# Kernel optimization log

Hardware: AMD Instinct MI355X
Metric: run time of the kernel (lower is better)

The kernel has to match this reference:

```python
import jax, jax.numpy as jnp
import numpy as np

RES = 128
NUM_SAMPLES = 64
EPS = 1e-8


def _trilinear_sample(vol, pts_norm):
    """Trilinear sample of vol [D,H,W] (D=H=W=RES) at pts_norm [N,3] in [-1,1],
    matching F.grid_sample(mode='bilinear', padding_mode='zeros', align_corners=True).
    pts_norm[...,0]=x indexes W, [...,1]=y indexes H, [...,2]=z indexes D."""
    R = vol.shape[0]
    flat = vol.reshape(-1)
    coords = (pts_norm + 1.0) * 0.5 * (R - 1)  # align_corners=True mapping
    x, y, z = coords[:, 0], coords[:, 1], coords[:, 2]
    x0 = jnp.floor(x); y0 = jnp.floor(y); z0 = jnp.floor(z)
    fx = x - x0; fy = y - y0; fz = z - z0

    def corner(xi, yi, zi, w):
        valid = (xi >= 0) & (xi < R) & (yi >= 0) & (yi < R) & (zi >= 0) & (zi < R)
        xc = jnp.clip(xi, 0, R - 1).astype(jnp.int32)
        yc = jnp.clip(yi, 0, R - 1).astype(jnp.int32)
        zc = jnp.clip(zi, 0, R - 1).astype(jnp.int32)
        vals = jnp.take(flat, zc * (R * R) + yc * R + xc)
        return jnp.where(valid, vals * w, 0.0)

    out = corner(x0, y0, z0, (1 - fx) * (1 - fy) * (1 - fz))
    out += corner(x0 + 1, y0, z0, fx * (1 - fy) * (1 - fz))
    out += corner(x0, y0 + 1, z0, (1 - fx) * fy * (1 - fz))
    out += corner(x0 + 1, y0 + 1, z0, fx * fy * (1 - fz))
    out += corner(x0, y0, z0 + 1, (1 - fx) * (1 - fy) * fz)
    out += corner(x0 + 1, y0, z0 + 1, fx * (1 - fy) * fz)
    out += corner(x0, y0 + 1, z0 + 1, (1 - fx) * fy * fz)
    out += corner(x0 + 1, y0 + 1, z0 + 1, fx * fy * fz)
    return out


def setup_inputs() -> dict:
    key = jax.random.key(0)
    voxel_volume = jax.random.normal(key, (1, 1, RES, RES, RES), dtype=jnp.float32)
    # 3DGS row-vector convention camera: world_view_transform = W2C^T
    cam_center = np.array([0.0, 0.0, -2.5], dtype=np.float32)
    w2c = np.eye(4, dtype=np.float32)
    w2c[:3, 3] = -cam_center  # identity rotation, camera looks along +z
    wvt = w2c.T.copy()
    # perspective projection (60 deg FOV), stored transposed (row convention)
    znear, zfar = 0.01, 100.0
    t = float(np.tan(np.deg2rad(30.0)))
    P = np.zeros((4, 4), dtype=np.float32)
    P[0, 0] = 1.0 / t
    P[1, 1] = 1.0 / t
    P[3, 2] = 1.0
    P[2, 2] = zfar / (zfar - znear)
    P[2, 3] = -(zfar * znear) / (zfar - znear)
    proj = P.T.copy()
    bbox = np.array([[-1.0, -1.0, -1.0], [1.0, 1.0, 1.0]], dtype=np.float32)
    return {
        "voxel_volume": voxel_volume,
        "world_view_transform": jnp.asarray(wvt),
        "projection_matrix": jnp.asarray(proj),
        "camera_center": jnp.asarray(cam_center),
        "bbox": jnp.asarray(bbox),
        "image_height": 512,
        "image_width": 512,
        "mode": 1,
    }


def reference(voxel_volume, world_view_transform, projection_matrix, camera_center,
              bbox, image_height, image_width, mode):
    H, W, S = int(image_height), int(image_width), NUM_SAMPLES
    vol = voxel_volume[0, 0]
    bbox_min, bbox_max = bbox[0], bbox[1]
    yy, xx = jnp.meshgrid(jnp.linspace(0.0, 1.0, H), jnp.linspace(0.0, 1.0, W), indexing="ij")
    ndc_x = xx * 2.0 - 1.0
    ndc_y = yy * 2.0 - 1.0
    view_inv = jnp.linalg.inv(world_view_transform)

    if mode == 0:
        # orthographic: rays parallel to -view z axis, origins on the image plane
        ray_dir = -view_inv[2, :3]
        ray_dir = ray_dir / (jnp.linalg.norm(ray_dir) + EPS)
        center = (bbox_min + bbox_max) / 2
        extent = bbox_max - bbox_min
        right = view_inv[0, :3]
        up = view_inv[1, :3]
        ray_origins = (center[None, None] + ndc_x[..., None] * right[None, None] * extent[0] / 2
                       + ndc_y[..., None] * up[None, None] * extent[1] / 2)
        diagonal = jnp.linalg.norm(extent)
        ray_origins = ray_origins - ray_dir * diagonal / 2
        ray_dirs = jnp.broadcast_to(ray_dir, (H, W, 3))
    else:
        # perspective: unproject NDC points through inverse projection + inverse view
        ray_origins = jnp.broadcast_to(camera_center, (H, W, 3))
        ones = jnp.ones_like(ndc_x)
        ndc_points = jnp.stack([ndc_x, ndc_y, ones, ones], axis=-1)  # [H,W,4]
        proj_inv = jnp.linalg.inv(projection_matrix)
        view_points = ndc_points @ proj_inv
        world_points = view_points @ view_inv
        world_points = world_points[..., :3] / (world_points[..., 3:4] + EPS)
        ray_dirs = world_points - ray_origins
        ray_dirs = ray_dirs / (jnp.linalg.norm(ray_dirs, axis=-1, keepdims=True) + EPS)

    # slab-method ray/box intersection (faithful: eps added to dirs, t_near clamped >= 0)
    inv_dir = 1.0 / (ray_dirs + EPS)
    t1 = (bbox_min - ray_origins) * inv_dir
    t2 = (bbox_max - ray_origins) * inv_dir
    t_near = jnp.max(jnp.minimum(t1, t2), axis=-1)
    t_far = jnp.min(jnp.maximum(t1, t2), axis=-1)
    t_near = jnp.maximum(t_near, 0.0)
    valid_mask = t_far > t_near

    t_vals = jnp.linspace(0.0, 1.0, S).reshape(1, 1, S)
    t_samples = t_near[..., None] + (t_far - t_near)[..., None] * t_vals       # [H,W,S]
    sample_points = ray_origins[..., None, :] + ray_dirs[..., None, :] * t_samples[..., None]  # [H,W,S,3]

    pts_norm = (sample_points - bbox_min) / (bbox_max - bbox_min + EPS) * 2.0 - 1.0
    sampled = _trilinear_sample(vol, pts_norm.reshape(-1, 3)).reshape(H, W, S)

    delta_t = (t_far - t_near) / S
    projection = (sampled * delta_t[..., None]).sum(axis=-1) * valid_mask.astype(jnp.float32)
    return projection[None]  # [1,H,W]
```

## Files before the change

kernel.cpp:

```cpp
#include <hip/hip_runtime.h>
#include <math.h>

#define RES 128
#define NS 64
#define EPSF 1e-8f
#define ZSL 8
#define NSLAB (RES / ZSL)
#define WXS 16
#define WYS 16
#define WROW 17
#define ZPL 9


__device__ void inv4x4(const float* __restrict__ A, double out[4][4]) {
    double m[4][8];
    for (int r = 0; r < 4; ++r) {
        for (int c = 0; c < 4; ++c) {
            m[r][c]     = (double)A[r * 4 + c];
            m[r][c + 4] = (r == c) ? 1.0 : 0.0;
        }
    }
    for (int col = 0; col < 4; ++col) {
        int piv = col;
        double best = fabs(m[col][col]);
        for (int r = col + 1; r < 4; ++r) {
            double v = fabs(m[r][col]);
            if (v > best) { best = v; piv = r; }
        }
        if (piv != col) {
            for (int c = 0; c < 8; ++c) {
                double t = m[col][c]; m[col][c] = m[piv][c]; m[piv][c] = t;
            }
        }
        double inv = 1.0 / m[col][col];
        for (int c = 0; c < 8; ++c) m[col][c] *= inv;
        for (int r = 0; r < 4; ++r) {
            if (r == col) continue;
            double f = m[r][col];
            for (int c = 0; c < 8; ++c) m[r][c] -= f * m[col][c];
        }
    }
    for (int r = 0; r < 4; ++r)
        for (int c = 0; c < 4; ++c)
            out[r][c] = m[r][c + 4];
}

__device__ __forceinline__ float2 load_f2(const float* __restrict__ p) {
    float2 r;
    __builtin_memcpy(&r, p, 8);
    return r;
}

__device__ __forceinline__ float cornerf(const float* __restrict__ vol,
                                         float xf, float yf, float zf, float w) {
    if (xf >= 0.f && xf <= 127.f &&
        yf >= 0.f && yf <= 127.f &&
        zf >= 0.f && zf <= 127.f) {
        int xi = (int)xf, yi = (int)yf, zi = (int)zf;
        return vol[(zi * RES + yi) * RES + xi] * w;
    }
    return 0.f;
}

__global__ __launch_bounds__(256) void dsv_render(
    const float* __restrict__ vol,
    const float* __restrict__ wvt,
    const float* __restrict__ proj,
    const float* __restrict__ cam,
    const float* __restrict__ bbox,
    const int*   __restrict__ pH,
    const int*   __restrict__ pW,
    const int*   __restrict__ pmode,
    float*       __restrict__ out)
{
    __shared__ float sC[28];
    __shared__ float crp[4][6];
    __shared__ int   win[NSLAB][2];
    __shared__ float slab[ZPL][WYS][WROW];

    const int H = pH[0];
    const int W = pW[0];
    const int mode = pmode[0];

    if (threadIdx.x == 0) {
        double vi[4][4], pinv[4][4];
        inv4x4(wvt, vi);
        inv4x4(proj, pinv);
        for (int i = 0; i < 4; ++i) {
            for (int j = 0; j < 4; ++j) {
                double s = 0.0;
                for (int k = 0; k < 4; ++k) s += pinv[i][k] * vi[k][j];
                sC[i * 4 + j] = (float)s;
            }
        }
        float bminx = bbox[0], bminy = bbox[1], bminz = bbox[2];
        float bmaxx = bbox[3], bmaxy = bbox[4], bmaxz = bbox[5];
        float ex = bmaxx - bminx, ey = bmaxy - bminy, ez = bmaxz - bminz;
        float ddx = -(float)vi[2][0], ddy = -(float)vi[2][1], ddz = -(float)vi[2][2];
        float nn = sqrtf(ddx * ddx + ddy * ddy + ddz * ddz) + EPSF;
        ddx /= nn; ddy /= nn; ddz /= nn;
        float diag = sqrtf(ex * ex + ey * ey + ez * ez);
        sC[16] = ddx; sC[17] = ddy; sC[18] = ddz;
        sC[19] = (float)vi[0][0] * ex * 0.5f;
        sC[20] = (float)vi[0][1] * ex * 0.5f;
        sC[21] = (float)vi[0][2] * ex * 0.5f;
        sC[22] = (float)vi[1][0] * ey * 0.5f;
        sC[23] = (float)vi[1][1] * ey * 0.5f;
        sC[24] = (float)vi[1][2] * ey * 0.5f;
        sC[25] = (bminx + bmaxx) * 0.5f - ddx * diag * 0.5f;
        sC[26] = (bminy + bmaxy) * 0.5f - ddy * diag * 0.5f;
        sC[27] = (bminz + bmaxz) * 0.5f - ddz * diag * 0.5f;
    }
    __syncthreads();

    const float bminx = bbox[0], bminy = bbox[1], bminz = bbox[2];
    const float bmaxx = bbox[3], bmaxy = bbox[4], bmaxz = bbox[5];
    const float kx = 127.0f / (bmaxx - bminx + EPSF);
    const float ky = 127.0f / (bmaxy - bminy + EPSF);
    const float kz = 127.0f / (bmaxz - bminz + EPSF);
    const float camx = cam[0], camy = cam[1], camz = cam[2];

    const int nTx = (W + 15) >> 4;
    const int nTy = (H + 15) >> 4;
    const int nTiles = nTx * nTy;
    const int tid = (int)threadIdx.x;
    const int tx = tid & 15;
    const int ty = tid >> 4;

    for (int tile = blockIdx.x; tile < nTiles; tile += gridDim.x) {
        const int ti = tile / nTx;
        const int tj = tile - ti * nTx;
        const int i = ti * 16 + ty;
        const int j = tj * 16 + tx;
        const bool inImg = (i < H) && (j < W);

        const float nx = (float)j / (float)(W - 1) * 2.0f - 1.0f;
        const float ny = (float)i / (float)(H - 1) * 2.0f - 1.0f;

        float ox, oy, oz, dx, dy, dz;
        if (mode == 0) {
            dx = sC[16]; dy = sC[17]; dz = sC[18];
            ox = sC[25] + nx * sC[19] + ny * sC[22];
            oy = sC[26] + nx * sC[20] + ny * sC[23];
            oz = sC[27] + nx * sC[21] + ny * sC[24];
        } else {
            float wx = nx * sC[0] + ny * sC[4] + sC[8]  + sC[12];
            float wy = nx * sC[1] + ny * sC[5] + sC[9]  + sC[13];
            float wz = nx * sC[2] + ny * sC[6] + sC[10] + sC[14];
            float ww = nx * sC[3] + ny * sC[7] + sC[11] + sC[15];
            float invw = 1.0f / (ww + EPSF);
            wx *= invw; wy *= invw; wz *= invw;
            ox = camx; oy = camy; oz = camz;
            dx = wx - ox; dy = wy - oy; dz = wz - oz;
            float n = sqrtf(dx * dx + dy * dy + dz * dz) + EPSF;
            dx /= n; dy /= n; dz /= n;
        }

        const float ix = 1.0f / (dx + EPSF);
        const float iy = 1.0f / (dy + EPSF);
        const float iz = 1.0f / (dz + EPSF);
        float t1 = (bminx - ox) * ix, t2 = (bmaxx - ox) * ix;
        float tn = fminf(t1, t2), tf = fmaxf(t1, t2);
        t1 = (bminy - oy) * iy; t2 = (bmaxy - oy) * iy;
        tn = fmaxf(tn, fminf(t1, t2)); tf = fminf(tf, fmaxf(t1, t2));
        t1 = (bminz - oz) * iz; t2 = (bmaxz - oz) * iz;
        tn = fmaxf(tn, fminf(t1, t2)); tf = fminf(tf, fmaxf(t1, t2));
        tn = fmaxf(tn, 0.0f);
        const bool valid = tf > tn;
        const float range = tf - tn;

        const float sdx = dx * kx, sdy = dy * ky, sdz = dz * kz;
        const float basex = fmaf(sdx, tn, (ox - bminx) * kx);
        const float basey = fmaf(sdy, tn, (oy - bminy) * ky);
        const float basez = fmaf(sdz, tn, (oz - bminz) * kz);
        const float r63 = range * (1.0f / 63.0f);
        const float qx = sdx * r63, qy = sdy * r63, qz = sdz * r63;

        int cidx = -1;
        if      (tid == 0)   cidx = 0;
        else if (tid == 15)  cidx = 1;
        else if (tid == 240) cidx = 2;
        else if (tid == 255) cidx = 3;
        if (cidx >= 0) {
            crp[cidx][0] = basex; crp[cidx][1] = basey; crp[cidx][2] = basez;
            crp[cidx][3] = qx;    crp[cidx][4] = qy;    crp[cidx][5] = qz;
        }
        __syncthreads();

        const bool ok = (mode != 0)
            && fabsf(crp[0][5]) > 1e-4f && fabsf(crp[1][5]) > 1e-4f
            && fabsf(crp[2][5]) > 1e-4f && fabsf(crp[3][5]) > 1e-4f;

        float sum = 0.0f;

        if (ok) {
            if (tid < NSLAB) {
                const float z0p = (float)(tid * ZSL);
                const float z1p = (float)(tid * ZSL + ZSL);
                float mnx = 1e30f, mny = 1e30f;
                #pragma unroll
                for (int c = 0; c < 4; ++c) {
                    const float bx = crp[c][0], by = crp[c][1], bz = crp[c][2];
                    const float cqx = crp[c][3], cqy = crp[c][4], cqz = crp[c][5];
                    const float iq = 1.0f / cqz;
                    const float s0 = (z0p - bz) * iq;
                    const float s1 = (z1p - bz) * iq;
                    const float xa = fmaf(cqx, s0, bx), xb = fmaf(cqx, s1, bx);
                    const float ya = fmaf(cqy, s0, by), yb = fmaf(cqy, s1, by);
                    mnx = fminf(mnx, fminf(xa, xb));
                    mny = fminf(mny, fminf(ya, yb));
                }
                mnx = fminf(fmaxf(mnx, -1e6f), 1e6f);
                mny = fminf(fmaxf(mny, -1e6f), 1e6f);
                win[tid][0] = (int)floorf(mnx) - 1;
                win[tid][1] = (int)floorf(mny) - 1;
            }

            int sc = 0;
            for (int k = 0; k < NSLAB; ++k) {
                __syncthreads();
                const int wx0 = win[k][0];
                const int wy0 = win[k][1];
                const int zk  = k * ZSL;

                {
                    const int gx = wx0 + tx, gy = wy0 + ty;
                    const bool lat = ((unsigned)gx < RES) && ((unsigned)gy < RES);
                    unsigned gaddr = (unsigned)((zk * RES + gy) * RES + gx);
                    #pragma unroll
                    for (int z = 0; z < ZPL; ++z) {
                        float v = 0.0f;
                        if (lat && (zk + z) < RES) v = vol[gaddr];
                        slab[z][ty][tx] = v;
                        gaddr += RES * RES;
                    }
                }
                __syncthreads();

                const float zend = (k == NSLAB - 1) ? 1e30f : (float)(zk + ZSL);

                while (sc < NS) {
                    const float fs = (float)sc;
                    const float cz = fmaf(qz, fs, basez);
                    if (!(cz < zend)) break;
                    const float cx = fmaf(qx, fs, basex);
                    const float cy = fmaf(qy, fs, basey);
                    const float x0f = floorf(cx), y0f = floorf(cy), z0f = floorf(cz);
                    const float fx = cx - x0f, fy = cy - y0f, fz = cz - z0f;
                    const int ix0 = (int)x0f, iy0 = (int)y0f, iz0 = (int)z0f;

                    if ((unsigned)(ix0 - wx0) <= (unsigned)(WXS - 2) &&
                        (unsigned)(iy0 - wy0) <= (unsigned)(WYS - 2) &&
                        (unsigned)(iz0 - zk)  <= (unsigned)(ZSL - 1) &&
                        x0f == x0f) {
                        const int lx = ix0 - wx0;
                        const int ly = iy0 - wy0;
                        const int lz = iz0 - zk;
                        const float* p = &slab[lz][ly][lx];
                        const float a00 = p[0],          a01 = p[1];
                        const float a10 = p[WROW],       a11 = p[WROW + 1];
                        const float b00 = p[WYS * WROW], b01 = p[WYS * WROW + 1];
                        const float b10 = p[WYS * WROW + WROW];
                        const float b11 = p[WYS * WROW + WROW + 1];
                        const float x00 = fmaf(fx, a01 - a00, a00);
                        const float x10 = fmaf(fx, a11 - a10, a10);
                        const float x01 = fmaf(fx, b01 - b00, b00);
                        const float x11 = fmaf(fx, b11 - b10, b10);
                        const float y0v = fmaf(fy, x10 - x00, x00);
                        const float y1v = fmaf(fy, x11 - x01, x01);
                        sum += fmaf(fz, y1v - y0v, y0v);
                    } else {
                        const float gxw = 1.0f - fx, gyw = 1.0f - fy, gzw = 1.0f - fz;
                        sum += cornerf(vol, x0f,       y0f,       z0f,       gxw * gyw * gzw);
                        sum += cornerf(vol, x0f + 1.f, y0f,       z0f,       fx  * gyw * gzw);
                        sum += cornerf(vol, x0f,       y0f + 1.f, z0f,       gxw * fy  * gzw);
                        sum += cornerf(vol, x0f + 1.f, y0f + 1.f, z0f,       fx  * fy  * gzw);
                        sum += cornerf(vol, x0f,       y0f,       z0f + 1.f, gxw * gyw * fz);
                        sum += cornerf(vol, x0f + 1.f, y0f,       z0f + 1.f, fx  * gyw * fz);
                        sum += cornerf(vol, x0f,       y0f + 1.f, z0f + 1.f, gxw * fy  * fz);
                        sum += cornerf(vol, x0f + 1.f, y0f + 1.f, z0f + 1.f, fx  * fy  * fz);
                    }
                    ++sc;
                }
            }
        } else {
            #pragma unroll 4
            for (int s = 0; s < NS; ++s) {
                const float fs = (float)s;
                const float cx = fmaf(qx, fs, basex);
                const float cy = fmaf(qy, fs, basey);
                const float cz = fmaf(qz, fs, basez);
                const float x0 = floorf(cx), y0 = floorf(cy), z0 = floorf(cz);
                const float fx = cx - x0, fy = cy - y0, fz = cz - z0;
                const float gx = 1.0f - fx, gy = 1.0f - fy, gz = 1.0f - fz;

                if (x0 >= 0.f && x0 <= 126.f &&
                    y0 >= 0.f && y0 <= 126.f &&
                    z0 >= 0.f && z0 <= 126.f) {
                    const int base = (((int)z0) * RES + ((int)y0)) * RES + ((int)x0);
                    const float2 vA = load_f2(vol + base);
                    const float2 vB = load_f2(vol + base + RES);
                    const float2 vC = load_f2(vol + base + RES * RES);
                    const float2 vD = load_f2(vol + base + RES * RES + RES);
                    const float gygz = gy * gz, fygz = fy * gz;
                    const float gyfz = gy * fz, fyfz = fy * fz;
                    sum += (vA.x * gx + vA.y * fx) * gygz
                         + (vB.x * gx + vB.y * fx) * fygz
                         + (vC.x * gx + vC.y * fx) * gyfz
                         + (vD.x * gx + vD.y * fx) * fyfz;
                } else {
                    sum += cornerf(vol, x0,       y0,       z0,       gx * gy * gz);
                    sum += cornerf(vol, x0 + 1.f, y0,       z0,       fx * gy * gz);
                    sum += cornerf(vol, x0,       y0 + 1.f, z0,       gx * fy * gz);
                    sum += cornerf(vol, x0 + 1.f, y0 + 1.f, z0,       fx * fy * gz);
                    sum += cornerf(vol, x0,       y0,       z0 + 1.f, gx * gy * fz);
                    sum += cornerf(vol, x0 + 1.f, y0,       z0 + 1.f, fx * gy * fz);
                    sum += cornerf(vol, x0,       y0 + 1.f, z0 + 1.f, gx * fy * fz);
                    sum += cornerf(vol, x0 + 1.f, y0 + 1.f, z0 + 1.f, fx * fy * fz);
                }
            }
        }

        if (inImg) {
            const float delta = range * (1.0f / 64.0f);
            out[i * W + j] = valid ? sum * delta : 0.0f;
        }
    }
}

extern "C" void kernel_launch(void* const* d_in, const int* in_sizes, int n_in,
                              void* d_out, int out_size, void* d_ws, size_t ws_size,
                              hipStream_t stream) {
    const float* vol  = (const float*)d_in[0];
    const float* wvt  = (const float*)d_in[1];
    const float* proj = (const float*)d_in[2];
    const float* cam  = (const float*)d_in[3];
    const float* bbox = (const float*)d_in[4];
    const int*   pH   = (const int*)d_in[5];
    const int*   pW   = (const int*)d_in[6];
    const int*   pmode= (const int*)d_in[7];
    float* out = (float*)d_out;

    int blocks = (out_size + 255) / 256;
    if (blocks < 1) blocks = 1;
    dsv_render<<<blocks, 256, 0, stream>>>(vol, wvt, proj, cam, bbox, pH, pW, pmode, out);
}
```

Measured before the change: 131.4 us.

## Prefetch next z-slab into registers while sampling current slab

Loads the next slab's voxels from global memory into registers before processing samples in the current slab, then writes them to shared memory after a barrier, so global load latency overlaps with the trilinear sampling work. The shared-memory corner reads are also changed to paired float2 loads. The change adds ZPL registers per thread and keeps two barriers per slab. load_f2 on the padded shared rows may produce misaligned 8-byte accesses.

```diff
diff --git a/kernel.cpp b/kernel.cpp
--- a/kernel.cpp
+++ b/kernel.cpp
@@ -215,27 +215,43 @@
                 win[tid][0] = (int)floorf(mnx) - 1;
                 win[tid][1] = (int)floorf(mny) - 1;
             }
+            __syncthreads();
+
+            float rv[ZPL];
+
+            {
+                const int wx0 = win[0][0], wy0 = win[0][1];
+                const int gx = wx0 + tx, gy = wy0 + ty;
+                const bool lat = ((unsigned)gx < RES) && ((unsigned)gy < RES);
+                unsigned gaddr = (unsigned)((gy * RES) + gx);
+                #pragma unroll
+                for (int z = 0; z < ZPL; ++z) {
+                    rv[z] = (lat && z < RES) ? vol[gaddr] : 0.0f;
+                    gaddr += RES * RES;
+                }
+                #pragma unroll
+                for (int z = 0; z < ZPL; ++z) slab[z][ty][tx] = rv[z];
+            }
+            __syncthreads();
 
             int sc = 0;
             for (int k = 0; k < NSLAB; ++k) {
-                __syncthreads();
                 const int wx0 = win[k][0];
                 const int wy0 = win[k][1];
                 const int zk  = k * ZSL;
 
-                {
-                    const int gx = wx0 + tx, gy = wy0 + ty;
+                if (k + 1 < NSLAB) {
+                    const int nzk = zk + ZSL;
+                    const int nwx0 = win[k + 1][0], nwy0 = win[k + 1][1];
+                    const int gx = nwx0 + tx, gy = nwy0 + ty;
                     const bool lat = ((unsigned)gx < RES) && ((unsigned)gy < RES);
-                    unsigned gaddr = (unsigned)((zk * RES + gy) * RES + gx);
+                    unsigned gaddr = (unsigned)(((nzk) * RES + gy) * RES + gx);
                     #pragma unroll
                     for (int z = 0; z < ZPL; ++z) {
-                        float v = 0.0f;
-                        if (lat && (zk + z) < RES) v = vol[gaddr];
-                        slab[z][ty][tx] = v;
+                        rv[z] = (lat && (nzk + z) < RES) ? vol[gaddr] : 0.0f;
                         gaddr += RES * RES;
                     }
                 }
-                __syncthreads();
 
                 const float zend = (k == NSLAB - 1) ? 1e30f : (float)(zk + ZSL);
 
@@ -257,15 +273,14 @@
                         const int ly = iy0 - wy0;
                         const int lz = iz0 - zk;
                         const float* p = &slab[lz][ly][lx];
-                        const float a00 = p[0],          a01 = p[1];
-                        const float a10 = p[WROW],       a11 = p[WROW + 1];
-                        const float b00 = p[WYS * WROW], b01 = p[WYS * WROW + 1];
-                        const float b10 = p[WYS * WROW + WROW];
-                        const float b11 = p[WYS * WROW + WROW + 1];
-                        const float x00 = fmaf(fx, a01 - a00, a00);
-                        const float x10 = fmaf(fx, a11 - a10, a10);
-                        const float x01 = fmaf(fx, b01 - b00, b00);
-                        const float x11 = fmaf(fx, b11 - b10, b10);
+                        const float2 A0 = load_f2(p);
+                        const float2 A1 = load_f2(p + WROW);
+                        const float2 B0 = load_f2(p + WYS * WROW);
+                        const float2 B1 = load_f2(p + WYS * WROW + WROW);
+                        const float x00 = fmaf(fx, A0.y - A0.x, A0.x);
+                        const float x10 = fmaf(fx, A1.y - A1.x, A1.x);
+                        const float x01 = fmaf(fx, B0.y - B0.x, B0.x);
+                        const float x11 = fmaf(fx, B1.y - B1.x, B1.x);
                         const float y0v = fmaf(fy, x10 - x00, x00);
                         const float y1v = fmaf(fy, x11 - x01, x01);
                         sum += fmaf(fz, y1v - y0v, y0v);
@@ -281,6 +296,13 @@
                         sum += cornerf(vol, x0f + 1.f, y0f + 1.f, z0f + 1.f, fx  * fy  * fz);
                     }
                     ++sc;
+                }
+
+                __syncthreads();
+                if (k + 1 < NSLAB) {
+                    #pragma unroll
+                    for (int z = 0; z < ZPL; ++z) slab[z][ty][tx] = rv[z];
+                    __syncthreads();
                 }
             }
         } else {
```

Measured after the change: 123.0 us. 1.07x faster.
